# Optimization experiments

Hardware: AMD Instinct MI355X
Metric: run time of the kernel (lower is better)

The kernel has to match this reference:

```python
import jax, jax.numpy as jnp
import numpy as np

ITEM_NUM = 100000
H = 128          # hidden_size
L_PROTO = 500    # number of prototypes
K = 4            # top-k prototypes
SEQ = 50         # max_seq_length
B = 1024
TAO = 0.1
LAMBDA = 0.1
EPS = 1e-5


def layer_norm(x, g, b):
    mu = jnp.mean(x, axis=-1, keepdims=True)
    var = jnp.mean((x - mu) ** 2, axis=-1, keepdims=True)
    return (x - mu) * jax.lax.rsqrt(var + EPS) * g + b


def setup_inputs() -> dict:
    key = jax.random.key(0)
    ks = jax.random.split(key, 12)
    std = 0.02
    item_emb = jax.random.normal(ks[0], (ITEM_NUM, H), jnp.float32) * std
    item_emb = item_emb.at[0].set(0.0)  # padding_idx=0
    pos_emb = jax.random.normal(ks[1], (SEQ + 1, H), jnp.float32) * std
    pos_emb = pos_emb.at[0].set(0.0)    # padding_idx=0 (never hit when len==SEQ)
    proto = jax.random.normal(ks[2], (L_PROTO, H), jnp.float32) * std
    w1 = jax.random.normal(ks[3], (H, H), jnp.float32) * std
    w2 = jax.random.normal(ks[4], (H, 1), jnp.float32) * std
    w3 = jax.random.normal(ks[5], (H, H), jnp.float32) * std
    w4 = jax.random.normal(ks[6], (H, H), jnp.float32) * std
    w5 = jax.random.normal(ks[7], (H, K), jnp.float32) * std
    w6 = jax.random.normal(ks[8], (H, H), jnp.float32) * std
    w7 = jax.random.normal(ks[9], (H, 1), jnp.float32) * std
    seq = jax.random.randint(ks[10], (B, SEQ), 0, ITEM_NUM, dtype=jnp.int64)
    g = jnp.ones((H,), jnp.float32)
    b = jnp.zeros((H,), jnp.float32)
    return {
        'item_emb': item_emb, 'pos_emb': pos_emb, 'proto': proto,
        'w1': w1, 'w2': w2, 'w3': w3, 'w4': w4, 'w5': w5, 'w6': w6, 'w7': w7,
        'ln1_g': g, 'ln1_b': b, 'ln2_g': g, 'ln2_b': b,
        'ln3_g': g, 'ln3_b': b, 'ln4_g': g, 'ln4_b': b,
        'seq': seq,
    }


def reference(item_emb, pos_emb, proto, w1, w2, w3, w4, w5, w6, w7,
              ln1_g, ln1_b, ln2_g, ln2_b, ln3_g, ln3_b, ln4_g, ln4_b, seq):
    mask = (seq != 0).astype(jnp.float32)            # [B,S]
    ie = item_emb[seq]                               # [B,S,H]

    # self-attentive virtual concept vector
    sa_score = jnp.squeeze(jnp.tanh(ie @ w1) @ w2, -1)   # [B,S]
    sa_score = sa_score - (1.0 - mask) * 10000.0
    alpha = jax.nn.softmax(sa_score, axis=-1)
    vcv = jnp.einsum('bs,bsh->bh', alpha, ie)            # [B,H]

    # prototype routing: top-k by score
    s = vcv @ proto.T                                    # [B,L]
    chosen_s, rank = jax.lax.top_k(s, K)                 # [B,K]
    chosen_proto = proto[rank]                           # [B,K,H]
    chosen_proto = jax.nn.sigmoid(chosen_s)[..., None] * chosen_proto

    # item->prototype assignment
    p_kt_score = jnp.einsum('bsh,bkh->bsk',
                            layer_norm(ie @ w3, ln1_g, ln1_b),
                            layer_norm(chosen_proto, ln2_g, ln2_b))
    p_kt = jax.nn.softmax(p_kt_score, axis=-1) * mask[:, :, None]  # [B,S,K]

    # positional embedding (positions SEQ..1)
    position = SEQ - jnp.arange(SEQ)                     # [S]
    emb = pos_emb[position][None, :, :] + ie             # [B,S,H]

    a_k_score = jnp.swapaxes(jnp.tanh(emb @ w4) @ w5, 1, 2)   # [B,K,S]
    a_k = jax.nn.softmax(a_k_score, axis=-1) * mask[:, None, :]
    a_k = jnp.swapaxes(a_k, 1, 2)                        # [B,S,K]

    p = p_kt * a_k
    interesting = layer_norm(jnp.einsum('bsk,bsh->bkh', p, emb), ln3_g, ln3_b)  # [B,K,H]

    xu = jnp.einsum('bsk,bkh->bsh', p_kt, chosen_proto)  # [B,S,H]
    c_score = jnp.squeeze(jnp.tanh(xu @ w6) @ w7, -1) - (1.0 - mask) * 10000.0
    c_w = jax.nn.softmax(c_score, axis=-1)               # [B,S]
    c_apt = layer_norm(jnp.einsum('bs,bsh->bh', c_w, xu), ln4_g, ln4_b)  # [B,H]

    e_score = jnp.einsum('bh,bkh->bk', c_apt, interesting)
    e = jax.nn.softmax(e_score / TAO, axis=-1)
    final = jnp.einsum('bk,bkh->bh', e, interesting)     # [B,H]
    scores = final @ item_emb.T                          # [B,ITEM_NUM]

    # prototype covariance regularizer
    centered = proto - jnp.mean(proto, axis=0, keepdims=True)
    M = (centered @ centered.T) / H
    Lc = (jnp.linalg.norm(M) - jnp.linalg.norm(jnp.diag(M))) * 0.5
    return scores, LAMBDA * Lc
```

## Files before the change

### kernel.cpp

```cpp
#include <hip/hip_runtime.h>
#include <hip/hip_bf16.h>

#define H 128
#define H2 132
#define SQL 50
#define LPROTO 500
#define KTOP 4
#define BQ 1024
#define ITEMS 100000

typedef __attribute__((ext_vector_type(8))) short bf16x8;
typedef __attribute__((ext_vector_type(4))) float f32x4;

__device__ __forceinline__ float wsum(float v){
#pragma unroll
  for (int o = 32; o; o >>= 1) v += __shfl_xor(v, o, 64);
  return v;
}
__device__ __forceinline__ float wmax(float v){
#pragma unroll
  for (int o = 32; o; o >>= 1) v = fmaxf(v, __shfl_xor(v, o, 64));
  return v;
}
__device__ __forceinline__ float gr16(float v){
  v += __shfl_xor(v, 1, 64);
  v += __shfl_xor(v, 2, 64);
  v += __shfl_xor(v, 4, 64);
  v += __shfl_xor(v, 8, 64);
  return v;
}
__device__ __forceinline__ unsigned short f2bf(float x){
  unsigned int u = __builtin_bit_cast(unsigned int, x);
  unsigned int r = u + 0x7fffu + ((u >> 16) & 1u);
  return (unsigned short)(r >> 16);
}
__device__ __forceinline__ float bf2f(unsigned short h){
  unsigned int u = ((unsigned int)h) << 16;
  return __builtin_bit_cast(float, u);
}
__device__ __forceinline__ float ftanh(float x){
  float e = __expf(-2.0f * fabsf(x));
  float t = (1.0f - e) / (1.0f + e);
  return copysignf(t, x);
}

__device__ __forceinline__ void mm_core(const float xs[4][8],
                                        const unsigned short* __restrict__ wt_hi,
                                        const unsigned short* __restrict__ wt_lo,
                                        int r15, int kof, f32x4* acc)
{
  bf16x8 ah[4], al[4];
#pragma unroll
  for (int ks = 0; ks < 4; ks++){
    bf16x8 h, l;
#pragma unroll
    for (int e = 0; e < 8; e++){
      unsigned short hb = f2bf(xs[ks][e]);
      float rem = xs[ks][e] - bf2f(hb);
      h[e] = (short)hb;
      l[e] = (short)f2bf(rem);
    }
    ah[ks] = h; al[ks] = l;
  }
#pragma unroll
  for (int j = 0; j < 8; j++){
    const unsigned short* bp = wt_hi + (j * 16 + r15) * H + kof;
    const unsigned short* lp = wt_lo + (j * 16 + r15) * H + kof;
    f32x4 a = (f32x4){0.f, 0.f, 0.f, 0.f};
#pragma unroll
    for (int ks = 0; ks < 4; ks++){
      bf16x8 bh = *reinterpret_cast<const bf16x8*>(bp + ks * 32);
      bf16x8 bl = *reinterpret_cast<const bf16x8*>(lp + ks * 32);
      a = __builtin_amdgcn_mfma_f32_16x16x32_bf16(ah[ks], bh, a, 0, 0, 0);
      a = __builtin_amdgcn_mfma_f32_16x16x32_bf16(al[ks], bh, a, 0, 0, 0);
      a = __builtin_amdgcn_mfma_f32_16x16x32_bf16(ah[ks], bl, a, 0, 0, 0);
    }
    acc[j] = a;
  }
}

__device__ __forceinline__ void mm_acc(const float (*src)[H2],
                                       const unsigned short* __restrict__ wt_hi,
                                       const unsigned short* __restrict__ wt_lo,
                                       int lane, int wave, f32x4* acc)
{
  const int r15 = lane & 15, g = lane >> 4, kof = g * 8;
  const int row = wave * 16 + r15;
  const int srw = (row < SQL) ? row : 0;
  float xs[4][8];
#pragma unroll
  for (int ks = 0; ks < 4; ks++){
    const float* p = &src[srw][ks * 32 + kof];
    float4 x0 = *reinterpret_cast<const float4*>(p);
    float4 x1 = *reinterpret_cast<const float4*>(p + 4);
    xs[ks][0]=x0.x; xs[ks][1]=x0.y; xs[ks][2]=x0.z; xs[ks][3]=x0.w;
    xs[ks][4]=x1.x; xs[ks][5]=x1.y; xs[ks][6]=x1.z; xs[ks][7]=x1.w;
  }
  mm_core(xs, wt_hi, wt_lo, r15, kof, acc);
}

__device__ __forceinline__ void mm_acc_pos(const float (*src)[H2],
                                           const float* __restrict__ pos_emb,
                                           const unsigned short* __restrict__ wt_hi,
                                           const unsigned short* __restrict__ wt_lo,
                                           int lane, int wave, f32x4* acc)
{
  const int r15 = lane & 15, g = lane >> 4, kof = g * 8;
  const int row = wave * 16 + r15;
  const int srw = (row < SQL) ? row : 0;
  const float* pp = pos_emb + (SQL - srw) * H;
  float xs[4][8];
#pragma unroll
  for (int ks = 0; ks < 4; ks++){
    const float* p = &src[srw][ks * 32 + kof];
    float4 x0 = *reinterpret_cast<const float4*>(p);
    float4 x1 = *reinterpret_cast<const float4*>(p + 4);
    float4 p0 = *reinterpret_cast<const float4*>(pp + ks * 32 + kof);
    float4 p1 = *reinterpret_cast<const float4*>(pp + ks * 32 + kof + 4);
    xs[ks][0]=x0.x+p0.x; xs[ks][1]=x0.y+p0.y; xs[ks][2]=x0.z+p0.z; xs[ks][3]=x0.w+p0.w;
    xs[ks][4]=x1.x+p1.x; xs[ks][5]=x1.y+p1.y; xs[ks][6]=x1.z+p1.z; xs[ks][7]=x1.w+p1.w;
  }
  mm_core(xs, wt_hi, wt_lo, r15, kof, acc);
}

extern "C" __global__ __launch_bounds__(256, 4)
void sine_row(const float* __restrict__ item_emb, const float* __restrict__ pos_emb,
              const float* __restrict__ proto,
              const float* __restrict__ w2, const float* __restrict__ w5,
              const float* __restrict__ w7,
              const unsigned short* __restrict__ wt,
              const float* __restrict__ ln1g, const float* __restrict__ ln1b,
              const float* __restrict__ ln2g, const float* __restrict__ ln2b,
              const float* __restrict__ ln3g, const float* __restrict__ ln3b,
              const float* __restrict__ ln4g, const float* __restrict__ ln4b,
              const int* __restrict__ seq,
              unsigned short* __restrict__ finalbf)
{
  __shared__ __align__(16) float sA[SQL][H2];
  __shared__ __align__(16) float scp[KTOP][H];
  __shared__ __align__(16) float slncp[KTOP][H];
  __shared__ __align__(16) float sintr[KTOP][H];
  __shared__ __align__(16) float svcv[H];
  __shared__ __align__(16) float scapt[H];
  __shared__ float srow[SQL];
  __shared__ float smask[SQL];
  __shared__ float spkt[SQL][KTOP];
  __shared__ float sak[SQL][KTOP];
  __shared__ float ssc[LPROTO];
  __shared__ float schs[KTOP];
  __shared__ int   srank[KTOP];
  __shared__ float sesc[KTOP];

  const int b = blockIdx.x;
  const int t = threadIdx.x;
  const int lane = t & 63;
  const int wave = t >> 6;
  const int r15 = lane & 15;
  const int g   = lane >> 4;
  const int* sq = seq + b * SQL;

  const unsigned short* w1t_hi = wt;
  const unsigned short* w1t_lo = wt + 16384;
  const unsigned short* w3t_hi = wt + 32768;
  const unsigned short* w3t_lo = wt + 49152;
  const unsigned short* w4t_hi = wt + 65536;
  const unsigned short* w4t_lo = wt + 81920;
  const unsigned short* w6t_hi = wt + 98304;
  const unsigned short* w6t_lo = wt + 114688;

  if (t < SQL) smask[t] = (sq[t] != 0) ? 1.0f : 0.0f;
  for (int c = t; c < SQL * (H / 4); c += 256){
    int s = c >> 5, q = c & 31;
    int idx = sq[s];
    float4 v = reinterpret_cast<const float4*>(item_emb)[idx * (H / 4) + q];
    reinterpret_cast<float4*>(&sA[s][0])[q] = v;
  }
  __syncthreads();

  {
    f32x4 acc[8];
    mm_acc(sA, w1t_hi, w1t_lo, lane, wave, acc);
    float p0 = 0.f, p1 = 0.f, p2 = 0.f, p3 = 0.f;
#pragma unroll
    for (int j = 0; j < 8; j++){
      float w2c = w2[j * 16 + r15];
      p0 = fmaf(ftanh(acc[j][0]), w2c, p0);
      p1 = fmaf(ftanh(acc[j][1]), w2c, p1);
      p2 = fmaf(ftanh(acc[j][2]), w2c, p2);
      p3 = fmaf(ftanh(acc[j][3]), w2c, p3);
    }
    p0 = gr16(p0); p1 = gr16(p1); p2 = gr16(p2); p3 = gr16(p3);
    if (r15 == 0){
      float pv[4] = {p0, p1, p2, p3};
#pragma unroll
      for (int r = 0; r < 4; r++){
        int orow = wave * 16 + g * 4 + r;
        if (orow < SQL) srow[orow] = pv[r] - (1.0f - smask[orow]) * 10000.0f;
      }
    }
  }
  __syncthreads();

  if (wave == 0){
    float v = (lane < SQL) ? srow[lane] : -1e30f;
    float m = wmax(v);
    float e = (lane < SQL) ? __expf(v - m) : 0.0f;
    float sum = wsum(e);
    if (lane < SQL) srow[lane] = e / sum;
  }
  __syncthreads();
  if (t < H){
    float acc = 0.f;
    for (int s = 0; s < SQL; s++) acc = fmaf(srow[s], sA[s][t], acc);
    svcv[t] = acc;
  }
  __syncthreads();

  for (int l = t; l < LPROTO; l += 256){
    const float4* pr = reinterpret_cast<const float4*>(proto + l * H);
    const float4* vc = reinterpret_cast<const float4*>(svcv);
    float acc = 0.f;
    for (int q = 0; q < H / 4; q++){
      float4 p = pr[q], v = vc[q];
      acc += p.x * v.x + p.y * v.y + p.z * v.z + p.w * v.w;
    }
    ssc[l] = acc;
  }
  __syncthreads();
  if (wave == 0){
    float cand[8];
#pragma unroll
    for (int i = 0; i < 8; i++){
      int l = lane + 64 * i;
      cand[i] = (l < LPROTO) ? ssc[l] : -1e30f;
    }
    for (int k = 0; k < KTOP; k++){
      float bv = -1e30f; int bi = 0x7fffffff;
#pragma unroll
      for (int i = 0; i < 8; i++){
        int l = lane + 64 * i;
        if (cand[i] > bv || (cand[i] == bv && l < bi)){ bv = cand[i]; bi = l; }
      }
#pragma unroll
      for (int o = 32; o; o >>= 1){
        float ov = __shfl_xor(bv, o, 64);
        int   oi = __shfl_xor(bi, o, 64);
        if (ov > bv || (ov == bv && oi < bi)){ bv = ov; bi = oi; }
      }
      if (lane == 0){ schs[k] = bv; srank[k] = bi; }
      int li = bi - lane;
#pragma unroll
      for (int i = 0; i < 8; i++) if (64 * i == li) cand[i] = -1e30f;
    }
  }
  __syncthreads();
  {
    int k = wave;
    int r = srank[k];
    float sg = 1.0f / (1.0f + __expf(-schs[k]));
    float v0 = sg * proto[r * H + lane];
    float v1 = sg * proto[r * H + 64 + lane];
    float mu = wsum(v0 + v1) * (1.0f / H);
    float d0 = v0 - mu, d1 = v1 - mu;
    float var = wsum(d0 * d0 + d1 * d1) * (1.0f / H);
    float rs = rsqrtf(var + 1e-5f);
    scp[k][lane] = v0; scp[k][64 + lane] = v1;
    slncp[k][lane]      = d0 * rs * ln2g[lane]      + ln2b[lane];
    slncp[k][64 + lane] = d1 * rs * ln2g[64 + lane] + ln2b[64 + lane];
  }
  __syncthreads();

  {
    f32x4 acc[8];
    mm_acc(sA, w3t_hi, w3t_lo, lane, wave, acc);
    float s0 = 0.f, s1 = 0.f, s2 = 0.f, s3 = 0.f;
#pragma unroll
    for (int j = 0; j < 8; j++){ s0 += acc[j][0]; s1 += acc[j][1]; s2 += acc[j][2]; s3 += acc[j][3]; }
    float mu0 = gr16(s0) * (1.0f / H), mu1 = gr16(s1) * (1.0f / H);
    float mu2 = gr16(s2) * (1.0f / H), mu3 = gr16(s3) * (1.0f / H);
    float q0 = 0.f, q1 = 0.f, q2 = 0.f, q3 = 0.f;
#pragma unroll
    for (int j = 0; j < 8; j++){
      float d0 = acc[j][0] - mu0, d1 = acc[j][1] - mu1;
      float d2 = acc[j][2] - mu2, d3 = acc[j][3] - mu3;
      q0 = fmaf(d0, d0, q0); q1 = fmaf(d1, d1, q1);
      q2 = fmaf(d2, d2, q2); q3 = fmaf(d3, d3, q3);
    }
    float rs0 = rsqrtf(gr16(q0) * (1.0f / H) + 1e-5f);
    float rs1 = rsqrtf(gr16(q1) * (1.0f / H) + 1e-5f);
    float rs2 = rsqrtf(gr16(q2) * (1.0f / H) + 1e-5f);
    float rs3 = rsqrtf(gr16(q3) * (1.0f / H) + 1e-5f);
    float pk[4][4];
#pragma unroll
    for (int k = 0; k < 4; k++)
#pragma unroll
      for (int r = 0; r < 4; r++) pk[k][r] = 0.f;
#pragma unroll
    for (int j = 0; j < 8; j++){
      int c = j * 16 + r15;
      float gg = ln1g[c], bb = ln1b[c];
      float l0 = fmaf((acc[j][0] - mu0) * rs0, gg, bb);
      float l1 = fmaf((acc[j][1] - mu1) * rs1, gg, bb);
      float l2 = fmaf((acc[j][2] - mu2) * rs2, gg, bb);
      float l3 = fmaf((acc[j][3] - mu3) * rs3, gg, bb);
#pragma unroll
      for (int k = 0; k < 4; k++){
        float w = slncp[k][c];
        pk[k][0] = fmaf(l0, w, pk[k][0]);
        pk[k][1] = fmaf(l1, w, pk[k][1]);
        pk[k][2] = fmaf(l2, w, pk[k][2]);
        pk[k][3] = fmaf(l3, w, pk[k][3]);
      }
    }
#pragma unroll
    for (int k = 0; k < 4; k++)
#pragma unroll
      for (int r = 0; r < 4; r++) pk[k][r] = gr16(pk[k][r]);
    if (r15 == 0){
#pragma unroll
      for (int r = 0; r < 4; r++){
        int orow = wave * 16 + g * 4 + r;
        if (orow < SQL){
          float m = fmaxf(fmaxf(pk[0][r], pk[1][r]), fmaxf(pk[2][r], pk[3][r]));
          float e0 = __expf(pk[0][r] - m), e1 = __expf(pk[1][r] - m);
          float e2 = __expf(pk[2][r] - m), e3 = __expf(pk[3][r] - m);
          float inv = 1.0f / (e0 + e1 + e2 + e3);
          float msk = smask[orow];
          spkt[orow][0] = e0 * inv * msk; spkt[orow][1] = e1 * inv * msk;
          spkt[orow][2] = e2 * inv * msk; spkt[orow][3] = e3 * inv * msk;
        }
      }
    }
  }
  __syncthreads();

  {
    f32x4 acc[8];
    mm_acc_pos(sA, pos_emb, w4t_hi, w4t_lo, lane, wave, acc);
    float pk[4][4];
#pragma unroll
    for (int k = 0; k < 4; k++)
#pragma unroll
      for (int r = 0; r < 4; r++) pk[k][r] = 0.f;
#pragma unroll
    for (int j = 0; j < 8; j++){
      int c = j * 16 + r15;
      float4 w5c = *reinterpret_cast<const float4*>(w5 + c * 4);
      float t0 = ftanh(acc[j][0]), t1 = ftanh(acc[j][1]);
      float t2 = ftanh(acc[j][2]), t3 = ftanh(acc[j][3]);
      pk[0][0] = fmaf(t0, w5c.x, pk[0][0]); pk[0][1] = fmaf(t1, w5c.x, pk[0][1]);
      pk[0][2] = fmaf(t2, w5c.x, pk[0][2]); pk[0][3] = fmaf(t3, w5c.x, pk[0][3]);
      pk[1][0] = fmaf(t0, w5c.y, pk[1][0]); pk[1][1] = fmaf(t1, w5c.y, pk[1][1]);
      pk[1][2] = fmaf(t2, w5c.y, pk[1][2]); pk[1][3] = fmaf(t3, w5c.y, pk[1][3]);
      pk[2][0] = fmaf(t0, w5c.z, pk[2][0]); pk[2][1] = fmaf(t1, w5c.z, pk[2][1]);
      pk[2][2] = fmaf(t2, w5c.z, pk[2][2]); pk[2][3] = fmaf(t3, w5c.z, pk[2][3]);
      pk[3][0] = fmaf(t0, w5c.w, pk[3][0]); pk[3][1] = fmaf(t1, w5c.w, pk[3][1]);
      pk[3][2] = fmaf(t2, w5c.w, pk[3][2]); pk[3][3] = fmaf(t3, w5c.w, pk[3][3]);
    }
#pragma unroll
    for (int k = 0; k < 4; k++)
#pragma unroll
      for (int r = 0; r < 4; r++) pk[k][r] = gr16(pk[k][r]);
    if (r15 == 0){
#pragma unroll
      for (int r = 0; r < 4; r++){
        int orow = wave * 16 + g * 4 + r;
        if (orow < SQL){
          sak[orow][0] = pk[0][r]; sak[orow][1] = pk[1][r];
          sak[orow][2] = pk[2][r]; sak[orow][3] = pk[3][r];
        }
      }
    }
  }
  __syncthreads();

  {
    int k = wave;
    float v = (lane < SQL) ? sak[lane][k] : -1e30f;
    float m = wmax(v);
    float e = (lane < SQL) ? __expf(v - m) : 0.0f;
    float sum = wsum(e);
    if (lane < SQL) sak[lane][k] = (e / sum) * smask[lane] * spkt[lane][k];
  }
  __syncthreads();

  for (int c = t; c < KTOP * H; c += 256){
    int k = c >> 7, h = c & 127;
    float acc = 0.f;
    for (int s = 0; s < SQL; s++)
      acc = fmaf(sak[s][k], sA[s][h] + pos_emb[(SQL - s) * H + h], acc);
    sintr[k][h] = acc;
  }
  __syncthreads();
  {
    int k = wave;
    float v0 = sintr[k][lane], v1 = sintr[k][64 + lane];
    float mu = wsum(v0 + v1) * (1.0f / H);
    float d0 = v0 - mu, d1 = v1 - mu;
    float var = wsum(d0 * d0 + d1 * d1) * (1.0f / H);
    float rs = rsqrtf(var + 1e-5f);
    sintr[k][lane]      = d0 * rs * ln3g[lane]      + ln3b[lane];
    sintr[k][64 + lane] = d1 * rs * ln3g[64 + lane] + ln3b[64 + lane];
  }
  __syncthreads();

  for (int c = t; c < SQL * H; c += 256){
    int s = c >> 7, h = c & 127;
    float acc = spkt[s][0] * scp[0][h] + spkt[s][1] * scp[1][h]
              + spkt[s][2] * scp[2][h] + spkt[s][3] * scp[3][h];
    sA[s][h] = acc;
  }
  __syncthreads();
  {
    f32x4 acc[8];
    mm_acc(sA, w6t_hi, w6t_lo, lane, wave, acc);
    float p0 = 0.f, p1 = 0.f, p2 = 0.f, p3 = 0.f;
#pragma unroll
    for (int j = 0; j < 8; j++){
      float w7c = w7[j * 16 + r15];
      p0 = fmaf(ftanh(acc[j][0]), w7c, p0);
      p1 = fmaf(ftanh(acc[j][1]), w7c, p1);
      p2 = fmaf(ftanh(acc[j][2]), w7c, p2);
      p3 = fmaf(ftanh(acc[j][3]), w7c, p3);
    }
    p0 = gr16(p0); p1 = gr16(p1); p2 = gr16(p2); p3 = gr16(p3);
    if (r15 == 0){
      float pv[4] = {p0, p1, p2, p3};
#pragma unroll
      for (int r = 0; r < 4; r++){
        int orow = wave * 16 + g * 4 + r;
        if (orow < SQL) srow[orow] = pv[r] - (1.0f - smask[orow]) * 10000.0f;
      }
    }
  }
  __syncthreads();

  if (wave == 0){
    float v = (lane < SQL) ? srow[lane] : -1e30f;
    float m = wmax(v);
    float e = (lane < SQL) ? __expf(v - m) : 0.0f;
    float sum = wsum(e);
    if (lane < SQL) srow[lane] = e / sum;
  }
  __syncthreads();
  if (t < H){
    float acc = 0.f;
    for (int s = 0; s < SQL; s++) acc = fmaf(srow[s], sA[s][t], acc);
    scapt[t] = acc;
  }
  __syncthreads();
  if (wave == 0){
    float v0 = scapt[lane], v1 = scapt[64 + lane];
    float mu = wsum(v0 + v1) * (1.0f / H);
    float d0 = v0 - mu, d1 = v1 - mu;
    float var = wsum(d0 * d0 + d1 * d1) * (1.0f / H);
    float rs = rsqrtf(var + 1e-5f);
    scapt[lane]      = d0 * rs * ln4g[lane]      + ln4b[lane];
    scapt[64 + lane] = d1 * rs * ln4g[64 + lane] + ln4b[64 + lane];
  }
  __syncthreads();

  {
    int k = wave;
    float part = scapt[lane] * sintr[k][lane] + scapt[64 + lane] * sintr[k][64 + lane];
    float sc = wsum(part);
    if (lane == 0) sesc[k] = sc;
  }
  __syncthreads();
  if (t < H){
    float e0 = sesc[0] * 10.0f, e1 = sesc[1] * 10.0f, e2 = sesc[2] * 10.0f, e3 = sesc[3] * 10.0f;
    float m = fmaxf(fmaxf(e0, e1), fmaxf(e2, e3));
    float x0 = __expf(e0 - m), x1 = __expf(e1 - m), x2 = __expf(e2 - m), x3 = __expf(e3 - m);
    float inv = 1.0f / (x0 + x1 + x2 + x3);
    float f = (x0 * sintr[0][t] + x1 * sintr[1][t] + x2 * sintr[2][t] + x3 * sintr[3][t]) * inv;
    finalbf[b * H + t] = f2bf(f);
  }
}

extern "C" __global__ void wprep(const float* __restrict__ w1, const float* __restrict__ w3,
                                 const float* __restrict__ w4, const float* __restrict__ w6,
                                 unsigned short* __restrict__ out){
  const float* srcs[4] = {w1, w3, w4, w6};
  const float* src = srcs[blockIdx.x];
  unsigned short* hi = out + blockIdx.x * 32768;
  unsigned short* lo = hi + 16384;
  for (int i = threadIdx.x; i < 16384; i += 256){
    int c = i >> 7, k = i & 127;
    float f = src[k * H + c];
    unsigned short h = f2bf(f);
    hi[i] = h;
    lo[i] = f2bf(f - bf2f(h));
  }
}

extern "C" __global__ void conv_bf16(const float* __restrict__ in,
                                     unsigned short* __restrict__ out, int n4){
  int i = blockIdx.x * blockDim.x + threadIdx.x;
  int stride = gridDim.x * blockDim.x;
  for (; i < n4; i += stride){
    float4 v = reinterpret_cast<const float4*>(in)[i];
    union { unsigned short u[4]; uint2 v2; } o;
    o.u[0] = f2bf(v.x); o.u[1] = f2bf(v.y); o.u[2] = f2bf(v.z); o.u[3] = f2bf(v.w);
    reinterpret_cast<uint2*>(out)[i] = o.v2;
  }
}

#define GBM 128
#define GBN 128
#define LDT 136

extern "C" __global__ __launch_bounds__(256)
void gemm_scores(const unsigned short* __restrict__ A,
                 const unsigned short* __restrict__ Bm,
                 float* __restrict__ C)
{
  __shared__ __align__(16) unsigned short sA[GBM][LDT];
  __shared__ __align__(16) unsigned short sB[GBN][LDT];
  const int t = threadIdx.x, lane = t & 63, wave = t >> 6;
  const int r15 = lane & 15, g = lane >> 4;
  const int n0 = blockIdx.x * GBN;
  const int m0 = blockIdx.y * GBM;

  for (int c = t; c < GBM * 16; c += 256){
    int r = c >> 4, q = c & 15;
    uint4 v = reinterpret_cast<const uint4*>(A + (m0 + r) * H)[q];
    *reinterpret_cast<uint4*>(&sA[r][q * 8]) = v;
  }
  for (int c = t; c < GBN * 16; c += 256){
    int r = c >> 4, q = c & 15;
    int n = n0 + r;
    uint4 v = make_uint4(0u, 0u, 0u, 0u);
    if (n < ITEMS) v = reinterpret_cast<const uint4*>(Bm + (size_t)n * H)[q];
    *reinterpret_cast<uint4*>(&sB[r][q * 8]) = v;
  }
  __syncthreads();

  const int wm = wave >> 1, wn = wave & 1;
  f32x4 acc[4][4];
#pragma unroll
  for (int i = 0; i < 4; i++)
#pragma unroll
    for (int j = 0; j < 4; j++) acc[i][j] = (f32x4){0.f, 0.f, 0.f, 0.f};

#pragma unroll
  for (int ks = 0; ks < 4; ks++){
    bf16x8 af[4], bfr[4];
#pragma unroll
    for (int i = 0; i < 4; i++)
      af[i] = *reinterpret_cast<const bf16x8*>(&sA[wm * 64 + i * 16 + r15][ks * 32 + g * 8]);
#pragma unroll
    for (int j = 0; j < 4; j++)
      bfr[j] = *reinterpret_cast<const bf16x8*>(&sB[wn * 64 + j * 16 + r15][ks * 32 + g * 8]);
#pragma unroll
    for (int i = 0; i < 4; i++)
#pragma unroll
      for (int j = 0; j < 4; j++)
        acc[i][j] = __builtin_amdgcn_mfma_f32_16x16x32_bf16(af[i], bfr[j], acc[i][j], 0, 0, 0);
  }

#pragma unroll
  for (int i = 0; i < 4; i++){
    int mrow = m0 + wm * 64 + i * 16 + g * 4;
#pragma unroll
    for (int j = 0; j < 4; j++){
      int ncol = n0 + wn * 64 + j * 16 + r15;
      if (ncol < ITEMS){
#pragma unroll
        for (int r = 0; r < 4; r++)
          C[(size_t)(mrow + r) * ITEMS + ncol] = acc[i][j][r];
      }
    }
  }
}

extern "C" __global__ void proto_mean(const float* __restrict__ proto,
                                      float* __restrict__ mean, float* __restrict__ accum){
  __shared__ float part[4][H];
  int t = threadIdx.x;
  int h = t & 127, p = t >> 7;
  if (t < 2) accum[t] = 0.0f;
  float acc = 0.f;
  for (int l = p; l < LPROTO; l += 4) acc += proto[l * H + h];
  part[p][h] = acc;
  __syncthreads();
  if (t < H) mean[t] = (part[0][t] + part[1][t] + part[2][t] + part[3][t]) * (1.0f / LPROTO);
}

extern "C" __global__ __launch_bounds__(256)
void proto_cov(const float* __restrict__ proto, const float* __restrict__ mean,
               float* __restrict__ accum){
  __shared__ float ci[H];
  __shared__ float cm[H];
  __shared__ float red[256];
  int i = blockIdx.x, t = threadIdx.x;
  if (t < H){ cm[t] = mean[t]; ci[t] = proto[i * H + t] - mean[t]; }
  __syncthreads();
  float total = 0.f;
  for (int j = t; j < LPROTO; j += 256){
    float acc = 0.f;
    for (int h = 0; h < H; h++) acc = fmaf(ci[h], proto[j * H + h] - cm[h], acc);
    float m = acc * (1.0f / H);
    total += m * m;
    if (j == i) atomicAdd(&accum[1], m * m);
  }
  red[t] = total; __syncthreads();
  for (int o = 128; o; o >>= 1){ if (t < o) red[t] += red[t + o]; __syncthreads(); }
  if (t == 0) atomicAdd(&accum[0], red[0]);
}

extern "C" __global__ void lc_final(const float* __restrict__ accum, float* __restrict__ out){
  out[(size_t)BQ * ITEMS] = 0.1f * 0.5f * (sqrtf(accum[0]) - sqrtf(accum[1]));
}

extern "C" void kernel_launch(void* const* d_in, const int* in_sizes, int n_in,
                              void* d_out, int out_size, void* d_ws, size_t ws_size,
                              hipStream_t stream){
  const float* item  = (const float*)d_in[0];
  const float* pos   = (const float*)d_in[1];
  const float* proto = (const float*)d_in[2];
  const float* w1 = (const float*)d_in[3];
  const float* w2 = (const float*)d_in[4];
  const float* w3 = (const float*)d_in[5];
  const float* w4 = (const float*)d_in[6];
  const float* w5 = (const float*)d_in[7];
  const float* w6 = (const float*)d_in[8];
  const float* w7 = (const float*)d_in[9];
  const float* ln1g = (const float*)d_in[10];
  const float* ln1b = (const float*)d_in[11];
  const float* ln2g = (const float*)d_in[12];
  const float* ln2b = (const float*)d_in[13];
  const float* ln3g = (const float*)d_in[14];
  const float* ln3b = (const float*)d_in[15];
  const float* ln4g = (const float*)d_in[16];
  const float* ln4b = (const float*)d_in[17];
  const int* seq = (const int*)d_in[18];
  float* out = (float*)d_out;

  char* ws = (char*)d_ws;
  float* accum = (float*)ws;
  float* mean  = (float*)(ws + 256);
  unsigned short* finalbf = (unsigned short*)(ws + 1024);
  unsigned short* itembf  = (unsigned short*)(ws + 263168);
  unsigned short* wtbuf   = (unsigned short*)(ws + 25863168);

  wprep<<<4, 256, 0, stream>>>(w1, w3, w4, w6, wtbuf);
  conv_bf16<<<2048, 256, 0, stream>>>(item, itembf, ITEMS * H / 4);

  sine_row<<<BQ, 256, 0, stream>>>(item, pos, proto, w2, w5, w7, wtbuf,
                                   ln1g, ln1b, ln2g, ln2b, ln3g, ln3b, ln4g, ln4b,
                                   seq, finalbf);

  gemm_scores<<<dim3((ITEMS + GBN - 1) / GBN, BQ / GBM), 256, 0, stream>>>(finalbf, itembf, out);

  proto_mean<<<1, 512, 0, stream>>>(proto, mean, accum);
  proto_cov<<<LPROTO, 256, 0, stream>>>(proto, mean, accum);
  lc_final<<<1, 1, 0, stream>>>(accum, out);
}
```

Measured before the change: 400.8 us.

## Remap GEMM tiles per XCD, transpose MFMA operands for vector stores, use tanhf

The scores GEMM now runs on a 1D grid whose block index is decoded so that each XCD gets a contiguous range of item tiles, with all batch tiles of a group of 14 item tiles on the same XCD to improve L2 reuse of item embeddings. The MFMA operands are swapped so that each lane holds four consecutive item columns, which allows 16-byte float4 stores to the large output instead of scalar strided stores. The custom fast tanh is replaced by the library tanhf, which is more accurate but may cost more instructions. The grid contains padded blocks that exit early.

```diff
diff --git a/kernel.cpp b/kernel.cpp
--- a/kernel.cpp
+++ b/kernel.cpp
@@ -37,11 +37,6 @@
 __device__ __forceinline__ float bf2f(unsigned short h){
   unsigned int u = ((unsigned int)h) << 16;
   return __builtin_bit_cast(float, u);
-}
-__device__ __forceinline__ float ftanh(float x){
-  float e = __expf(-2.0f * fabsf(x));
-  float t = (1.0f - e) / (1.0f + e);
-  return copysignf(t, x);
 }
 
 __device__ __forceinline__ void mm_core(const float xs[4][8],
@@ -184,10 +179,10 @@
 #pragma unroll
     for (int j = 0; j < 8; j++){
       float w2c = w2[j * 16 + r15];
-      p0 = fmaf(ftanh(acc[j][0]), w2c, p0);
-      p1 = fmaf(ftanh(acc[j][1]), w2c, p1);
-      p2 = fmaf(ftanh(acc[j][2]), w2c, p2);
-      p3 = fmaf(ftanh(acc[j][3]), w2c, p3);
+      p0 = fmaf(tanhf(acc[j][0]), w2c, p0);
+      p1 = fmaf(tanhf(acc[j][1]), w2c, p1);
+      p2 = fmaf(tanhf(acc[j][2]), w2c, p2);
+      p3 = fmaf(tanhf(acc[j][3]), w2c, p3);
     }
     p0 = gr16(p0); p1 = gr16(p1); p2 = gr16(p2); p3 = gr16(p3);
     if (r15 == 0){
@@ -346,8 +341,8 @@
     for (int j = 0; j < 8; j++){
       int c = j * 16 + r15;
       float4 w5c = *reinterpret_cast<const float4*>(w5 + c * 4);
-      float t0 = ftanh(acc[j][0]), t1 = ftanh(acc[j][1]);
-      float t2 = ftanh(acc[j][2]), t3 = ftanh(acc[j][3]);
+      float t0 = tanhf(acc[j][0]), t1 = tanhf(acc[j][1]);
+      float t2 = tanhf(acc[j][2]), t3 = tanhf(acc[j][3]);
       pk[0][0] = fmaf(t0, w5c.x, pk[0][0]); pk[0][1] = fmaf(t1, w5c.x, pk[0][1]);
       pk[0][2] = fmaf(t2, w5c.x, pk[0][2]); pk[0][3] = fmaf(t3, w5c.x, pk[0][3]);
       pk[1][0] = fmaf(t0, w5c.y, pk[1][0]); pk[1][1] = fmaf(t1, w5c.y, pk[1][1]);
@@ -418,10 +413,10 @@
 #pragma unroll
     for (int j = 0; j < 8; j++){
       float w7c = w7[j * 16 + r15];
-      p0 = fmaf(ftanh(acc[j][0]), w7c, p0);
-      p1 = fmaf(ftanh(acc[j][1]), w7c, p1);
-      p2 = fmaf(ftanh(acc[j][2]), w7c, p2);
-      p3 = fmaf(ftanh(acc[j][3]), w7c, p3);
+      p0 = fmaf(tanhf(acc[j][0]), w7c, p0);
+      p1 = fmaf(tanhf(acc[j][1]), w7c, p1);
+      p2 = fmaf(tanhf(acc[j][2]), w7c, p2);
+      p3 = fmaf(tanhf(acc[j][3]), w7c, p3);
     }
     p0 = gr16(p0); p1 = gr16(p1); p2 = gr16(p2); p3 = gr16(p3);
     if (r15 == 0){
@@ -508,18 +503,29 @@
 #define GBM 128
 #define GBN 128
 #define LDT 136
+#define NTILES 782
 
 extern "C" __global__ __launch_bounds__(256)
 void gemm_scores(const unsigned short* __restrict__ A,
                  const unsigned short* __restrict__ Bm,
                  float* __restrict__ C)
 {
+  const int X = blockIdx.x;
+  const int xcd = X & 7;
+  const int slot = X >> 3;
+  const int chunk = slot / 112;
+  const int rem = slot % 112;
+  const int mt = rem / 14;
+  const int nl = rem % 14;
+  const int nt = xcd * 98 + chunk * 14 + nl;
+  if (nt >= NTILES) return;
+  const int n0 = nt * GBN;
+  const int m0 = mt * GBM;
+
   __shared__ __align__(16) unsigned short sA[GBM][LDT];
   __shared__ __align__(16) unsigned short sB[GBN][LDT];
   const int t = threadIdx.x, lane = t & 63, wave = t >> 6;
   const int r15 = lane & 15, g = lane >> 4;
-  const int n0 = blockIdx.x * GBN;
-  const int m0 = blockIdx.y * GBM;
 
   for (int c = t; c < GBM * 16; c += 256){
     int r = c >> 4, q = c & 15;
@@ -547,10 +553,10 @@
     bf16x8 af[4], bfr[4];
 #pragma unroll
     for (int i = 0; i < 4; i++)
-      af[i] = *reinterpret_cast<const bf16x8*>(&sA[wm * 64 + i * 16 + r15][ks * 32 + g * 8]);
+      af[i] = *reinterpret_cast<const bf16x8*>(&sB[wn * 64 + i * 16 + r15][ks * 32 + g * 8]);
 #pragma unroll
     for (int j = 0; j < 4; j++)
-      bfr[j] = *reinterpret_cast<const bf16x8*>(&sB[wn * 64 + j * 16 + r15][ks * 32 + g * 8]);
+      bfr[j] = *reinterpret_cast<const bf16x8*>(&sA[wm * 64 + j * 16 + r15][ks * 32 + g * 8]);
 #pragma unroll
     for (int i = 0; i < 4; i++)
 #pragma unroll
@@ -560,14 +566,12 @@
 
 #pragma unroll
   for (int i = 0; i < 4; i++){
-    int mrow = m0 + wm * 64 + i * 16 + g * 4;
-#pragma unroll
-    for (int j = 0; j < 4; j++){
-      int ncol = n0 + wn * 64 + j * 16 + r15;
-      if (ncol < ITEMS){
-#pragma unroll
-        for (int r = 0; r < 4; r++)
-          C[(size_t)(mrow + r) * ITEMS + ncol] = acc[i][j][r];
+    int item = n0 + wn * 64 + i * 16 + g * 4;
+    if (item < ITEMS){
+#pragma unroll
+      for (int j = 0; j < 4; j++){
+        int batch = m0 + wm * 64 + j * 16 + r15;
+        *reinterpret_cast<f32x4*>(C + (size_t)batch * ITEMS + item) = acc[i][j];
       }
     }
   }
@@ -650,7 +654,7 @@
                                    ln1g, ln1b, ln2g, ln2b, ln3g, ln3b, ln4g, ln4b,
                                    seq, finalbf);
 
-  gemm_scores<<<dim3((ITEMS + GBN - 1) / GBN, BQ / GBM), 256, 0, stream>>>(finalbf, itembf, out);
+  gemm_scores<<<dim3(6272), 256, 0, stream>>>(finalbf, itembf, out);
 
   proto_mean<<<1, 512, 0, stream>>>(proto, mean, accum);
   proto_cov<<<LPROTO, 256, 0, stream>>>(proto, mean, accum);
```

New measurement: 436.8 us. +9.0%, slower.
